# Performance work log

Measured on AMD Instinct MI355X. Metric: run time of the kernel, lower is better.

Reference implementation:

```python
import jax, jax.numpy as jnp
import numpy as np

HEADS = 12
HEAD_SIZE = 64
NEG_BIG = 1e12


def _rope_sincos(n, head_size, dtype):
    # rotary position embeddings: (n, head_size) each, with each freq repeated twice
    pos = jnp.arange(n, dtype=dtype)
    inv = jnp.power(10000.0, -2.0 * jnp.arange(head_size // 2, dtype=dtype) / head_size)
    emb = pos[:, None] * inv[None, :]               # (n, head_size//2)
    sin = jnp.repeat(jnp.sin(emb), 2, axis=-1)       # (n, head_size)
    cos = jnp.repeat(jnp.cos(emb), 2, axis=-1)
    return sin, cos


def _rotate_half(x):
    # stack([-x[...,1::2], x[...,::2]], -1).reshape_as(x)
    x2 = jnp.stack([-x[..., 1::2], x[..., ::2]], axis=-1)
    return x2.reshape(x.shape)


def setup_inputs() -> dict:
    key = jax.random.key(0)
    k1, k2, k3 = jax.random.split(key, 3)
    b, n, h = 16, 512, 1024
    inputs = jax.random.normal(k1, (b, n, h), dtype=jnp.float32)
    attention_mask = jnp.ones((b, n), dtype=jnp.float32)
    W1 = jax.random.normal(k2, (h, 2 * HEAD_SIZE), dtype=jnp.float32) * (1.0 / np.sqrt(h))
    b1 = jnp.zeros((2 * HEAD_SIZE,), dtype=jnp.float32)
    W2 = jax.random.normal(k3, (2 * HEAD_SIZE, 2 * HEADS), dtype=jnp.float32) * (1.0 / np.sqrt(2 * HEAD_SIZE))
    b2 = jnp.zeros((2 * HEADS,), dtype=jnp.float32)
    return {"inputs": inputs, "attention_mask": attention_mask,
            "W1": W1, "b1": b1, "W2": W2, "b2": b2}


def reference(inputs, attention_mask, W1, b1, W2, b2):
    b, n, _ = inputs.shape
    x = inputs @ W1 + b1                              # (b, n, 2*head_size)
    qw, kw = x[..., ::2], x[..., 1::2]                # (b, n, head_size)

    sin, cos = _rope_sincos(n, HEAD_SIZE, x.dtype)    # (n, head_size)
    qw = qw * cos[None] + _rotate_half(qw) * sin[None]
    kw = kw * cos[None] + _rotate_half(kw) * sin[None]

    logits = jnp.einsum('bmd,bnd->bmn', qw, kw) / (HEAD_SIZE ** 0.5)  # (b, n, n)

    bias = (x @ W2 + b2).transpose(0, 2, 1) / 2.0     # (b, 2*heads, n)
    logits = logits[:, None] + bias[:, ::2, None, :] + bias[:, 1::2, :, None]  # (b, heads, n, n)

    attn = 1.0 - attention_mask[:, None, None, :] * attention_mask[:, None, :, None]
    logits = logits - attn * NEG_BIG

    tril = jnp.tril(jnp.ones((n, n), dtype=logits.dtype), k=-1)
    logits = logits - tril[None, None] * NEG_BIG
    return logits
```

## Files before the change

kernel.cpp:

```cpp
#include <hip/hip_runtime.h>
#include <math.h>

#define NB 16
#define SEQ 512
#define HID 1024
#define XDIM 128
#define NHEADS 12
#define NROWS (NB*SEQ)
#define NEG_BIG 1000000000000.0f
#define MTILE 16

typedef __bf16 bf16x8 __attribute__((ext_vector_type(8)));
typedef __bf16 bf16x4 __attribute__((ext_vector_type(4)));
typedef float  f32x4  __attribute__((ext_vector_type(4)));

__global__ __launch_bounds__(256) void egp_prep(
    const float* __restrict__ W1, __bf16* __restrict__ W1T)
{
    int idx = blockIdx.x * 256 + threadIdx.x;
    int n   = idx >> 7;
    int k0  = (idx & 127) << 3;
    bf16x8 o;
    #pragma unroll
    for (int j = 0; j < 8; j++)
        o[j] = (__bf16)W1[(size_t)(k0 + j) * XDIM + n];
    *(bf16x8*)(W1T + (size_t)n * HID + k0) = o;
}

__global__ __launch_bounds__(256) void egp_stage1(
    const float* __restrict__ inp,
    const __bf16* __restrict__ W1T,
    const float* __restrict__ b1,
    const float* __restrict__ W2,
    const float* __restrict__ b2,
    float* __restrict__ qw,
    float* __restrict__ kw,
    float* __restrict__ biasw)
{
    __shared__ __bf16 As[2048];
    __shared__ float  Xs[MTILE][132];
    __shared__ float  W2s[XDIM * 24];
    __shared__ float  b2s[24];

    const int t    = threadIdx.x;
    const int row0 = blockIdx.x * MTILE;
    const int lane = t & 63;
    const int w    = t >> 6;
    const int quad = lane >> 4;
    const int mrow = lane & 15;
    const int ncol0 = w * 32;

    for (int i = t; i < XDIM * 24; i += 256) W2s[i] = W2[i];
    if (t < 24) b2s[t] = b2[t];

    const int m_st = t >> 4;
    const int k_st = (t & 15) * 4;
    const int s_st  = k_st >> 5;
    const int q_st  = (k_st & 31) >> 3;
    const int j_st  = k_st & 7;
    const int off_st = s_st * 1024 + q_st * 128 + m_st * 8 + j_st;
    const float* aptr = inp + (size_t)(row0 + m_st) * HID + k_st;

    f32x4 acc0 = {0.f, 0.f, 0.f, 0.f};
    f32x4 acc1 = {0.f, 0.f, 0.f, 0.f};

    float4 v = *(const float4*)(aptr);

    for (int kc = 0; kc < HID; kc += 64) {
        __syncthreads();
        bf16x4 p;
        p[0] = (__bf16)v.x; p[1] = (__bf16)v.y;
        p[2] = (__bf16)v.z; p[3] = (__bf16)v.w;
        *(bf16x4*)(&As[off_st]) = p;
        __syncthreads();
        if (kc + 64 < HID) v = *(const float4*)(aptr + kc + 64);

        #pragma unroll
        for (int s2 = 0; s2 < 2; s2++) {
            bf16x8 a = *(bf16x8*)(&As[s2 * 1024 + quad * 128 + mrow * 8]);
            {
                const __bf16* bp = W1T + (size_t)(ncol0 + mrow) * HID
                                 + kc + s2 * 32 + quad * 8;
                bf16x8 b = *(const bf16x8*)(bp);
                acc0 = __builtin_amdgcn_mfma_f32_16x16x32_bf16(a, b, acc0, 0, 0, 0);
            }
            {
                const __bf16* bp = W1T + (size_t)(ncol0 + 16 + mrow) * HID
                                 + kc + s2 * 32 + quad * 8;
                bf16x8 b = *(const bf16x8*)(bp);
                acc1 = __builtin_amdgcn_mfma_f32_16x16x32_bf16(a, b, acc1, 0, 0, 0);
            }
        }
    }

    float b1v0 = b1[ncol0 + mrow];
    float b1v1 = b1[ncol0 + 16 + mrow];
    #pragma unroll
    for (int r = 0; r < 4; r++) {
        Xs[quad * 4 + r][ncol0 + mrow]      = acc0[r] + b1v0;
        Xs[quad * 4 + r][ncol0 + 16 + mrow] = acc1[r] + b1v1;
    }
    __syncthreads();

    const int tx = t & 15;
    const int r  = t >> 4;
    const float LOG1E4 = 9.210340371976184f;
    float inv0 = expf(-((float)(2 * tx)     * (1.0f / 32.0f)) * LOG1E4);
    float inv1 = expf(-((float)(2 * tx + 1) * (1.0f / 32.0f)) * LOG1E4);
    {
        int grow  = row0 + r;
        float pos = (float)(grow & (SEQ - 1));
        float x[8];
        #pragma unroll
        for (int j = 0; j < 8; j++) x[j] = Xs[r][tx * 8 + j];
        float s0 = sinf(pos * inv0), c0 = cosf(pos * inv0);
        float s1 = sinf(pos * inv1), c1 = cosf(pos * inv1);
        float4 q4, k4;
        q4.x = x[0] * c0 - x[2] * s0;
        q4.y = x[2] * c0 + x[0] * s0;
        q4.z = x[4] * c1 - x[6] * s1;
        q4.w = x[6] * c1 + x[4] * s1;
        k4.x = x[1] * c0 - x[3] * s0;
        k4.y = x[3] * c0 + x[1] * s0;
        k4.z = x[5] * c1 - x[7] * s1;
        k4.w = x[7] * c1 + x[5] * s1;
        *(float4*)(qw + (size_t)grow * 64 + tx * 4) = q4;
        *(float4*)(kw + (size_t)grow * 64 + tx * 4) = k4;
    }

    for (int o = t; o < MTILE * 24; o += 256) {
        int row = o / 24;
        int jj  = o - row * 24;
        float s = 0.0f;
        for (int kk = 0; kk < XDIM; kk++)
            s += Xs[row][kk] * W2s[kk * 24 + jj];
        biasw[(size_t)(row0 + row) * 24 + jj] = (s + b2s[jj]) * 0.5f;
    }
}

__global__ __launch_bounds__(256) void egp_stage2(
    const float* __restrict__ qw,
    const float* __restrict__ kw,
    const float* __restrict__ biasw,
    const float* __restrict__ am,
    float* __restrict__ out)
{
    __shared__ float Qs[64][68];
    __shared__ float Ks[64][68];
    __shared__ float bEs[12][64];
    __shared__ float bOs[12][64];
    __shared__ float amN[64];
    __shared__ float amM[64];

    const int b  = blockIdx.z;
    const int m0 = blockIdx.y * 64;
    const int n0 = blockIdx.x * 64;
    const int t  = threadIdx.x;
    const int tx = t & 15;
    const int ty = t >> 4;

    #pragma unroll
    for (int j = 0; j < 4; j++) {
        int f4 = t + 256 * j;
        int r  = f4 >> 4;
        int c  = (f4 & 15) << 2;
        *(float4*)(&Qs[r][c]) = *(const float4*)(qw + (size_t)(b * SEQ + m0 + r) * 64 + c);
        *(float4*)(&Ks[r][c]) = *(const float4*)(kw + (size_t)(b * SEQ + n0 + r) * 64 + c);
    }
    for (int o = t; o < 768; o += 256) {
        int nn = o & 63;
        int h  = o >> 6;
        bEs[h][nn] = biasw[(size_t)(b * SEQ + n0 + nn) * 24 + 2 * h];
        bOs[h][nn] = biasw[(size_t)(b * SEQ + m0 + nn) * 24 + 2 * h + 1];
    }
    if (t < 64)       amN[t]      = am[b * SEQ + n0 + t];
    else if (t < 128) amM[t - 64] = am[b * SEQ + m0 + (t - 64)];
    __syncthreads();

    float acc[4][4];
    #pragma unroll
    for (int i = 0; i < 4; i++)
        #pragma unroll
        for (int j = 0; j < 4; j++) acc[i][j] = 0.0f;

    for (int k = 0; k < 64; k += 4) {
        float4 qv[4], kv[4];
        #pragma unroll
        for (int i = 0; i < 4; i++) qv[i] = *(const float4*)(&Qs[ty * 4 + i][k]);
        #pragma unroll
        for (int j = 0; j < 4; j++) kv[j] = *(const float4*)(&Ks[tx * 4 + j][k]);
        #pragma unroll
        for (int i = 0; i < 4; i++)
            #pragma unroll
            for (int j = 0; j < 4; j++)
                acc[i][j] += qv[i].x * kv[j].x + qv[i].y * kv[j].y
                           + qv[i].z * kv[j].z + qv[i].w * kv[j].w;
    }

    float amMv[4], amNv[4];
    #pragma unroll
    for (int i = 0; i < 4; i++) amMv[i] = amM[ty * 4 + i];
    #pragma unroll
    for (int j = 0; j < 4; j++) amNv[j] = amN[tx * 4 + j];

    float vals[4][4];
    #pragma unroll
    for (int i = 0; i < 4; i++) {
        int m = m0 + ty * 4 + i;
        #pragma unroll
        for (int j = 0; j < 4; j++) {
            int n = n0 + tx * 4 + j;
            float msk = (1.0f - amMv[i] * amNv[j]) * NEG_BIG
                      + ((n < m) ? NEG_BIG : 0.0f);
            vals[i][j] = acc[i][j] * 0.125f - msk;
        }
    }

    for (int h = 0; h < NHEADS; h++) {
        float be[4], bo[4];
        #pragma unroll
        for (int j = 0; j < 4; j++) be[j] = bEs[h][tx * 4 + j];
        #pragma unroll
        for (int i = 0; i < 4; i++) bo[i] = bOs[h][ty * 4 + i];
        float* obase = out + ((size_t)((b * NHEADS + h) * SEQ + m0 + ty * 4)) * SEQ + n0 + tx * 4;
        #pragma unroll
        for (int i = 0; i < 4; i++) {
            float4 o4;
            o4.x = vals[i][0] + be[0] + bo[i];
            o4.y = vals[i][1] + be[1] + bo[i];
            o4.z = vals[i][2] + be[2] + bo[i];
            o4.w = vals[i][3] + be[3] + bo[i];
            *(float4*)(obase + (size_t)i * SEQ) = o4;
        }
    }
}

extern "C" void kernel_launch(void* const* d_in, const int* in_sizes, int n_in,
                              void* d_out, int out_size, void* d_ws, size_t ws_size,
                              hipStream_t stream) {
    const float* inp = (const float*)d_in[0];
    const float* am  = (const float*)d_in[1];
    const float* W1  = (const float*)d_in[2];
    const float* b1  = (const float*)d_in[3];
    const float* W2  = (const float*)d_in[4];
    const float* b2  = (const float*)d_in[5];
    float* out = (float*)d_out;

    float* qw   = (float*)d_ws;
    float* kw   = qw + (size_t)NROWS * 64;
    float* bias = kw + (size_t)NROWS * 64;
    __bf16* w1t = (__bf16*)(bias + (size_t)NROWS * 24);

    egp_prep<<<64, 256, 0, stream>>>(W1, w1t);
    egp_stage1<<<NROWS / MTILE, 256, 0, stream>>>(inp, w1t, b1, W2, b2, qw, kw, bias);

    dim3 g2(SEQ / 64, SEQ / 64, NB);
    egp_stage2<<<g2, 256, 0, stream>>>(qw, kw, bias, am, out);
}
```

Before: 263.8 us.

## Store q/k as bf16 and compute stage2 QK^T with MFMA; prefetch all input chunks

Stage1 now writes the rotary-embedded q and k in bf16 instead of fp32, and loads all sixteen 64-wide chunks of its input row into registers up front rather than one chunk ahead. Stage2 replaces the scalar fp32 shared-memory dot-product loop with bf16 MFMA 16x16x32 instructions that read q and k directly from global memory. The MFMA results pass through a shared tile before the existing mask, bias and store epilogue. This trades fp32 precision in the logits for fewer ALU cycles and less q/k traffic, and adds register pressure from the 16-deep prefetch in stage1.

After: 265.6 us. About the same (+0.7%).

```diff
diff --git a/kernel.cpp b/kernel.cpp
--- a/kernel.cpp
+++ b/kernel.cpp
@@ -33,8 +33,8 @@
     const float* __restrict__ b1,
     const float* __restrict__ W2,
     const float* __restrict__ b2,
-    float* __restrict__ qw,
-    float* __restrict__ kw,
+    __bf16* __restrict__ qw,
+    __bf16* __restrict__ kw,
     float* __restrict__ biasw)
 {
     __shared__ __bf16 As[2048];
@@ -61,19 +61,23 @@
     const int off_st = s_st * 1024 + q_st * 128 + m_st * 8 + j_st;
     const float* aptr = inp + (size_t)(row0 + m_st) * HID + k_st;
 
+    float4 v[16];
+    #pragma unroll
+    for (int c = 0; c < 16; c++)
+        v[c] = *(const float4*)(aptr + 64 * c);
+
     f32x4 acc0 = {0.f, 0.f, 0.f, 0.f};
     f32x4 acc1 = {0.f, 0.f, 0.f, 0.f};
 
-    float4 v = *(const float4*)(aptr);
-
-    for (int kc = 0; kc < HID; kc += 64) {
+    #pragma unroll
+    for (int c = 0; c < 16; c++) {
+        const int kc = c * 64;
         __syncthreads();
         bf16x4 p;
-        p[0] = (__bf16)v.x; p[1] = (__bf16)v.y;
-        p[2] = (__bf16)v.z; p[3] = (__bf16)v.w;
+        p[0] = (__bf16)v[c].x; p[1] = (__bf16)v[c].y;
+        p[2] = (__bf16)v[c].z; p[3] = (__bf16)v[c].w;
         *(bf16x4*)(&As[off_st]) = p;
         __syncthreads();
-        if (kc + 64 < HID) v = *(const float4*)(aptr + kc + 64);
 
         #pragma unroll
         for (int s2 = 0; s2 < 2; s2++) {
@@ -115,17 +119,17 @@
         for (int j = 0; j < 8; j++) x[j] = Xs[r][tx * 8 + j];
         float s0 = sinf(pos * inv0), c0 = cosf(pos * inv0);
         float s1 = sinf(pos * inv1), c1 = cosf(pos * inv1);
-        float4 q4, k4;
-        q4.x = x[0] * c0 - x[2] * s0;
-        q4.y = x[2] * c0 + x[0] * s0;
-        q4.z = x[4] * c1 - x[6] * s1;
-        q4.w = x[6] * c1 + x[4] * s1;
-        k4.x = x[1] * c0 - x[3] * s0;
-        k4.y = x[3] * c0 + x[1] * s0;
-        k4.z = x[5] * c1 - x[7] * s1;
-        k4.w = x[7] * c1 + x[5] * s1;
-        *(float4*)(qw + (size_t)grow * 64 + tx * 4) = q4;
-        *(float4*)(kw + (size_t)grow * 64 + tx * 4) = k4;
+        bf16x4 q4, k4;
+        q4[0] = (__bf16)(x[0] * c0 - x[2] * s0);
+        q4[1] = (__bf16)(x[2] * c0 + x[0] * s0);
+        q4[2] = (__bf16)(x[4] * c1 - x[6] * s1);
+        q4[3] = (__bf16)(x[6] * c1 + x[4] * s1);
+        k4[0] = (__bf16)(x[1] * c0 - x[3] * s0);
+        k4[1] = (__bf16)(x[3] * c0 + x[1] * s0);
+        k4[2] = (__bf16)(x[5] * c1 - x[7] * s1);
+        k4[3] = (__bf16)(x[7] * c1 + x[5] * s1);
+        *(bf16x4*)(qw + (size_t)grow * 64 + tx * 4) = q4;
+        *(bf16x4*)(kw + (size_t)grow * 64 + tx * 4) = k4;
     }
 
     for (int o = t; o < MTILE * 24; o += 256) {
@@ -139,14 +143,13 @@
 }
 
 __global__ __launch_bounds__(256) void egp_stage2(
-    const float* __restrict__ qw,
-    const float* __restrict__ kw,
+    const __bf16* __restrict__ qw,
+    const __bf16* __restrict__ kw,
     const float* __restrict__ biasw,
     const float* __restrict__ am,
     float* __restrict__ out)
 {
-    __shared__ float Qs[64][68];
-    __shared__ float Ks[64][68];
+    __shared__ float Vals[64][68];
     __shared__ float bEs[12][64];
     __shared__ float bOs[12][64];
     __shared__ float amN[64];
@@ -156,17 +159,11 @@
     const int m0 = blockIdx.y * 64;
     const int n0 = blockIdx.x * 64;
     const int t  = threadIdx.x;
-    const int tx = t & 15;
-    const int ty = t >> 4;
-
-    #pragma unroll
-    for (int j = 0; j < 4; j++) {
-        int f4 = t + 256 * j;
-        int r  = f4 >> 4;
-        int c  = (f4 & 15) << 2;
-        *(float4*)(&Qs[r][c]) = *(const float4*)(qw + (size_t)(b * SEQ + m0 + r) * 64 + c);
-        *(float4*)(&Ks[r][c]) = *(const float4*)(kw + (size_t)(b * SEQ + n0 + r) * 64 + c);
-    }
+    const int lane = t & 63;
+    const int w    = t >> 6;
+    const int quad = lane >> 4;
+    const int l16  = lane & 15;
+
     for (int o = t; o < 768; o += 256) {
         int nn = o & 63;
         int h  = o >> 6;
@@ -175,27 +172,32 @@
     }
     if (t < 64)       amN[t]      = am[b * SEQ + n0 + t];
     else if (t < 128) amM[t - 64] = am[b * SEQ + m0 + (t - 64)];
+
+    const __bf16* qbase = qw + ((size_t)(b * SEQ + m0 + w * 16 + l16)) * 64 + quad * 8;
+    bf16x8 a0 = *(const bf16x8*)(qbase);
+    bf16x8 a1 = *(const bf16x8*)(qbase + 32);
+
+    f32x4 acc[4];
+    #pragma unroll
+    for (int nt = 0; nt < 4; nt++) {
+        const __bf16* kbase = kw + ((size_t)(b * SEQ + n0 + nt * 16 + l16)) * 64 + quad * 8;
+        bf16x8 b0 = *(const bf16x8*)(kbase);
+        bf16x8 b1 = *(const bf16x8*)(kbase + 32);
+        f32x4 z = {0.f, 0.f, 0.f, 0.f};
+        z = __builtin_amdgcn_mfma_f32_16x16x32_bf16(a0, b0, z, 0, 0, 0);
+        z = __builtin_amdgcn_mfma_f32_16x16x32_bf16(a1, b1, z, 0, 0, 0);
+        acc[nt] = z;
+    }
+
+    #pragma unroll
+    for (int nt = 0; nt < 4; nt++)
+        #pragma unroll
+        for (int r = 0; r < 4; r++)
+            Vals[w * 16 + quad * 4 + r][nt * 16 + l16] = acc[nt][r];
     __syncthreads();
 
-    float acc[4][4];
-    #pragma unroll
-    for (int i = 0; i < 4; i++)
-        #pragma unroll
-        for (int j = 0; j < 4; j++) acc[i][j] = 0.0f;
-
-    for (int k = 0; k < 64; k += 4) {
-        float4 qv[4], kv[4];
-        #pragma unroll
-        for (int i = 0; i < 4; i++) qv[i] = *(const float4*)(&Qs[ty * 4 + i][k]);
-        #pragma unroll
-        for (int j = 0; j < 4; j++) kv[j] = *(const float4*)(&Ks[tx * 4 + j][k]);
-        #pragma unroll
-        for (int i = 0; i < 4; i++)
-            #pragma unroll
-            for (int j = 0; j < 4; j++)
-                acc[i][j] += qv[i].x * kv[j].x + qv[i].y * kv[j].y
-                           + qv[i].z * kv[j].z + qv[i].w * kv[j].w;
-    }
+    const int tx = t & 15;
+    const int ty = t >> 4;
 
     float amMv[4], amNv[4];
     #pragma unroll
@@ -207,12 +209,14 @@
     #pragma unroll
     for (int i = 0; i < 4; i++) {
         int m = m0 + ty * 4 + i;
+        float4 v4 = *(const float4*)(&Vals[ty * 4 + i][tx * 4]);
+        float qk[4] = {v4.x, v4.y, v4.z, v4.w};
         #pragma unroll
         for (int j = 0; j < 4; j++) {
             int n = n0 + tx * 4 + j;
             float msk = (1.0f - amMv[i] * amNv[j]) * NEG_BIG
                       + ((n < m) ? NEG_BIG : 0.0f);
-            vals[i][j] = acc[i][j] * 0.125f - msk;
+            vals[i][j] = qk[j] * 0.125f - msk;
         }
     }
 
@@ -246,10 +250,10 @@
     const float* b2  = (const float*)d_in[5];
     float* out = (float*)d_out;
 
-    float* qw   = (float*)d_ws;
-    float* kw   = qw + (size_t)NROWS * 64;
-    float* bias = kw + (size_t)NROWS * 64;
-    __bf16* w1t = (__bf16*)(bias + (size_t)NROWS * 24);
+    __bf16* qw   = (__bf16*)d_ws;
+    __bf16* kw   = qw + (size_t)NROWS * 64;
+    float*  bias = (float*)(kw + (size_t)NROWS * 64);
+    __bf16* w1t  = (__bf16*)(bias + (size_t)NROWS * 24);
 
     egp_prep<<<64, 256, 0, stream>>>(W1, w1t);
     egp_stage1<<<NROWS / MTILE, 256, 0, stream>>>(inp, w1t, b1, W2, b2, qw, kw, bias);
```
